# Optimization experiments

Measured on AMD Instinct MI355X. Metric: run time of the kernel, lower is better.

The kernel has to match this reference:

```python
import jax, jax.numpy as jnp
import numpy as np

N = 100000      # nodes
E = 1600000     # edges (avg degree 16)
IN, HID, OUT = 256, 256, 128


def setup_inputs() -> dict:
    key = jax.random.key(0)
    ks = jax.random.split(key, 9)
    x = jax.random.normal(ks[0], (N, IN), jnp.float32)
    edge_index = jax.random.randint(ks[1], (2, E), 0, N, dtype=jnp.int64)
    perm = jax.random.permutation(ks[2], N).astype(jnp.int64)
    # GCN layer params (glorot-ish scale) and Bilinear discriminator params
    W1 = jax.random.normal(ks[3], (IN, HID), jnp.float32) * (1.0 / np.sqrt(IN))
    b1 = jnp.zeros((HID,), jnp.float32)
    W2 = jax.random.normal(ks[4], (HID, OUT), jnp.float32) * (1.0 / np.sqrt(HID))
    b2 = jnp.zeros((OUT,), jnp.float32)
    Wb = jax.random.normal(ks[5], (OUT, OUT), jnp.float32) * (1.0 / np.sqrt(OUT))
    bb = jnp.zeros((1,), jnp.float32)
    return {"x": x, "edge_index": edge_index, "perm": perm,
            "W1": W1, "b1": b1, "W2": W2, "b2": b2, "Wb": Wb, "bb": bb}


def reference(x, edge_index, perm, W1, b1, W2, b2, Wb, bb):
    n = x.shape[0]
    src, dst = edge_index[0], edge_index[1]
    # GCN symmetric norm with self-loops: deg = 1 + in-degree
    deg = 1.0 + jax.ops.segment_sum(jnp.ones(src.shape[0], x.dtype), dst,
                                    num_segments=n)
    dinv = jax.lax.rsqrt(deg)                 # [N]
    enorm = dinv[src] * dinv[dst]             # per-edge norm
    self_norm = dinv * dinv                   # self-loop norm

    def gcn(h, W, b):
        hw = h @ W                                            # [N, F]
        agg = jax.ops.segment_sum(hw[src] * enorm[:, None], dst,
                                  num_segments=n)             # scatter-add
        return agg + self_norm[:, None] * hw + b

    def encode(h):
        return gcn(jax.nn.relu(gcn(h, W1, b1)), W2, b2)       # [N, OUT]

    H = encode(x)
    s = jax.nn.sigmoid(H.mean(axis=0))                        # summary [OUT]

    def disc(Hh):
        # nn.Bilinear(d, d, 1): score_n = H_n^T Wb s + bb
        return (jnp.einsum('nd,de,e->n', Hh, Wb, s) + bb)[:, None]

    pos_scores = disc(H)
    neg_scores = disc(encode(x[perm]))
    return pos_scores, neg_scores
```

## Files before the change

### kernel.cpp

```cpp
#include <hip/hip_runtime.h>


typedef __attribute__((ext_vector_type(8))) short bh8;
typedef __attribute__((ext_vector_type(4))) float f4;
typedef __attribute__((ext_vector_type(4))) unsigned short u16x4;

#define AS1 __attribute__((address_space(1)))
#define AS3 __attribute__((address_space(3)))

__device__ __forceinline__ unsigned short f2b(float f) {
    unsigned int u = __float_as_uint(f);
    unsigned int r = (u + 0x7FFFu + ((u >> 16) & 1u)) >> 16;
    return (unsigned short)r;
}
__device__ __forceinline__ float b2f(unsigned short h) {
    return __uint_as_float(((unsigned int)h) << 16);
}

__global__ void k_degree(const int* __restrict__ dst, int* __restrict__ deg, int E) {
    int e = blockIdx.x * blockDim.x + threadIdx.x;
    if (e < E) atomicAdd(&deg[dst[e]], 1);
}

__global__ void k_dinv(const int* __restrict__ deg, float* __restrict__ dinv,
                       int* __restrict__ rowptr, int N, int E) {
    int n = blockIdx.x * blockDim.x + threadIdx.x;
    if (n < N) dinv[n] = 1.0f / sqrtf(1.0f + (float)deg[n]);
    if (n == 0) rowptr[N] = E;
}

__global__ void k_scanA(const int* __restrict__ in, int* __restrict__ out,
                        int* __restrict__ bsum, int n) {
    __shared__ int sh[256];
    int t = threadIdx.x;
    int base = blockIdx.x * 1024 + t * 4;
    int v[4];
#pragma unroll
    for (int j = 0; j < 4; ++j) v[j] = (base + j < n) ? in[base + j] : 0;
    int s = v[0] + v[1] + v[2] + v[3];
    sh[t] = s;
    __syncthreads();
    for (int off = 1; off < 256; off <<= 1) {
        int u = (t >= off) ? sh[t - off] : 0;
        __syncthreads();
        sh[t] += u;
        __syncthreads();
    }
    int excl = sh[t] - s;
    if (t == 255) bsum[blockIdx.x] = sh[255];
    int run = excl;
#pragma unroll
    for (int j = 0; j < 4; ++j) {
        if (base + j < n) out[base + j] = run;
        run += v[j];
    }
}

__global__ void k_scanB(const int* __restrict__ bsum, int* __restrict__ boff, int nb) {
    __shared__ int sh[128];
    int t = threadIdx.x;
    int v = (t < nb) ? bsum[t] : 0;
    sh[t] = v;
    __syncthreads();
    for (int off = 1; off < 128; off <<= 1) {
        int u = (t >= off) ? sh[t - off] : 0;
        __syncthreads();
        sh[t] += u;
        __syncthreads();
    }
    boff[t] = sh[t] - v;
}

__global__ void k_scanC(int* __restrict__ out, const int* __restrict__ boff, int n) {
    int t = threadIdx.x;
    int base = blockIdx.x * 1024 + t * 4;
    int add = boff[blockIdx.x];
#pragma unroll
    for (int j = 0; j < 4; ++j)
        if (base + j < n) out[base + j] += add;
}

__global__ void k_fill(const int* __restrict__ src, const int* __restrict__ dst,
                       const int* __restrict__ perm, const int* __restrict__ rowptr,
                       int* __restrict__ cursor, int* __restrict__ csr,
                       int* __restrict__ pcsr, int E) {
    int e = blockIdx.x * blockDim.x + threadIdx.x;
    if (e >= E) return;
    int d = dst[e];
    int s = src[e];
    int p = rowptr[d] + atomicAdd(&cursor[d], 1);
    csr[p] = s;
    pcsr[p] = perm[s];
}

__global__ void k_split(const float* __restrict__ in, unsigned short* __restrict__ hi,
                        unsigned short* __restrict__ lo, long n4) {
    long i = (long)blockIdx.x * blockDim.x + threadIdx.x;
    if (i >= n4) return;
    float4 v = ((const float4*)in)[i];
    float f[4] = {v.x, v.y, v.z, v.w};
    u16x4 h, l;
#pragma unroll
    for (int j = 0; j < 4; ++j) {
        unsigned short hb = f2b(f[j]);
        h[j] = hb;
        l[j] = f2b(f[j] - b2f(hb));
    }
    ((u16x4*)hi)[i] = h;
    ((u16x4*)lo)[i] = l;
}

__global__ void k_wsplitT(const float* __restrict__ W, unsigned short* __restrict__ thi,
                          unsigned short* __restrict__ tlo, int K, int Nc) {
    int t = blockIdx.x * blockDim.x + threadIdx.x;
    if (t >= K * Nc) return;
    int k = t / Nc, n = t % Nc;
    float f = W[t];
    unsigned short hb = f2b(f);
    thi[n * K + k] = hb;
    tlo[n * K + k] = f2b(f - b2f(hb));
}

__global__ __launch_bounds__(256, 2) void k_gemm_mfma(
        const unsigned short* __restrict__ Ahi0, const unsigned short* __restrict__ Alo0,
        const unsigned short* __restrict__ Ahi1, const unsigned short* __restrict__ Alo1,
        const unsigned short* __restrict__ Bhi, const unsigned short* __restrict__ Blo,
        unsigned short* __restrict__ C, int M, int K, int NcB, int ldC, int colz) {
    __shared__ short lds[4][128 * 32];
    const int tid  = threadIdx.x;
    const int lane = tid & 63;
    const int w    = tid >> 6;
    const int wr   = w >> 1, wc = w & 1;
    const int row0 = blockIdx.y * 128;
    const int bcol = blockIdx.x * 128;
    const unsigned short* Ahi = blockIdx.z ? Ahi1 : Ahi0;
    const unsigned short* Alo = blockIdx.z ? Alo1 : Alo0;

    const unsigned short* sp = (w == 0) ? Ahi : (w == 1) ? Alo : (w == 2) ? Bhi : Blo;
    const int  base0 = (w < 2) ? row0 : bcol;
    const int  lim   = (w < 2) ? (M - 1) : (NcB - 1);
    const int  rsub  = lane >> 2;
    const int  clin  = lane & 3;

    f4 acc[4][4] = {};

    for (int k0 = 0; k0 < K; k0 += 32) {
        __syncthreads();
#pragma unroll
        for (int s = 0; s < 8; ++s) {
            int r = s * 16 + rsub;
            int g = base0 + r;
            if (g > lim) g = lim;
            const unsigned short* srcp = sp + (size_t)g * K + k0 + clin * 8;
            __builtin_amdgcn_global_load_lds((const AS1 void*)srcp,
                                             (AS3 void*)&lds[w][s * 512], 16, 0, 0);
        }
        __syncthreads();

        bh8 ah[4], al[4], bh_[4], bl[4];
        const int fr = lane & 15;
        const int fc = (lane >> 4) * 8;
#pragma unroll
        for (int m = 0; m < 4; ++m) {
            int off = (wr * 64 + m * 16 + fr) * 32 + fc;
            ah[m] = *(const bh8*)&lds[0][off];
            al[m] = *(const bh8*)&lds[1][off];
        }
#pragma unroll
        for (int n = 0; n < 4; ++n) {
            int off = (wc * 64 + n * 16 + fr) * 32 + fc;
            bh_[n] = *(const bh8*)&lds[2][off];
            bl[n]  = *(const bh8*)&lds[3][off];
        }
#pragma unroll
        for (int m = 0; m < 4; ++m)
#pragma unroll
            for (int n = 0; n < 4; ++n)
                acc[m][n] = __builtin_amdgcn_mfma_f32_16x16x32_bf16(ah[m], bh_[n], acc[m][n], 0, 0, 0);
#pragma unroll
        for (int m = 0; m < 4; ++m)
#pragma unroll
            for (int n = 0; n < 4; ++n)
                acc[m][n] = __builtin_amdgcn_mfma_f32_16x16x32_bf16(ah[m], bl[n], acc[m][n], 0, 0, 0);
#pragma unroll
        for (int m = 0; m < 4; ++m)
#pragma unroll
            for (int n = 0; n < 4; ++n)
                acc[m][n] = __builtin_amdgcn_mfma_f32_16x16x32_bf16(al[m], bh_[n], acc[m][n], 0, 0, 0);
    }

    const int cr = (lane >> 4) * 4;
    const int cc = lane & 15;
    const int col0 = bcol + blockIdx.z * colz;
#pragma unroll
    for (int m = 0; m < 4; ++m) {
        int r0 = row0 + wr * 64 + m * 16 + cr;
#pragma unroll
        for (int n = 0; n < 4; ++n) {
            int c = col0 + wc * 64 + n * 16 + cc;
#pragma unroll
            for (int j = 0; j < 4; ++j) {
                int r = r0 + j;
                if (r < M) C[(size_t)r * ldC + c] = f2b(acc[m][n][j]);
            }
        }
    }
}

__global__ __launch_bounds__(256) void k_agg2(
        const unsigned short* __restrict__ hw, const int* __restrict__ rowptr,
        const int* __restrict__ csr, const int* __restrict__ pcsr,
        const int* __restrict__ perm, const float* __restrict__ dinv,
        const float* __restrict__ bias,
        unsigned short* __restrict__ pos_hi, unsigned short* __restrict__ pos_lo,
        unsigned short* __restrict__ neg_hi, unsigned short* __restrict__ neg_lo,
        int n) {
    int wid = (blockIdx.x * blockDim.x + threadIdx.x) >> 6;
    int lane = threadIdx.x & 63;
    if (wid >= n) return;
    float dn = dinv[wid];
    int beg = rowptr[wid], end = rowptr[wid + 1];
    int off = lane * 4;
    float ap[4] = {0.f, 0.f, 0.f, 0.f}, an[4] = {0.f, 0.f, 0.f, 0.f};
    int e = beg;
    for (; e + 3 < end; e += 4) {
        int s0 = csr[e],     s1 = csr[e + 1], s2 = csr[e + 2], s3 = csr[e + 3];
        int p0 = pcsr[e],    p1 = pcsr[e + 1], p2 = pcsr[e + 2], p3 = pcsr[e + 3];
        float w0 = dinv[s0], w1 = dinv[s1],   w2 = dinv[s2],   w3 = dinv[s3];
        u16x4 vp0 = *(const u16x4*)(hw + (size_t)s0 * 256 + off);
        u16x4 vp1 = *(const u16x4*)(hw + (size_t)s1 * 256 + off);
        u16x4 vp2 = *(const u16x4*)(hw + (size_t)s2 * 256 + off);
        u16x4 vp3 = *(const u16x4*)(hw + (size_t)s3 * 256 + off);
        u16x4 vn0 = *(const u16x4*)(hw + (size_t)p0 * 256 + off);
        u16x4 vn1 = *(const u16x4*)(hw + (size_t)p1 * 256 + off);
        u16x4 vn2 = *(const u16x4*)(hw + (size_t)p2 * 256 + off);
        u16x4 vn3 = *(const u16x4*)(hw + (size_t)p3 * 256 + off);
#pragma unroll
        for (int j = 0; j < 4; ++j) {
            ap[j] += (w0 * b2f(vp0[j]) + w1 * b2f(vp1[j]))
                   + (w2 * b2f(vp2[j]) + w3 * b2f(vp3[j]));
            an[j] += (w0 * b2f(vn0[j]) + w1 * b2f(vn1[j]))
                   + (w2 * b2f(vn2[j]) + w3 * b2f(vn3[j]));
        }
    }
    for (; e < end; ++e) {
        int s0 = csr[e];
        int p0 = pcsr[e];
        float w0 = dinv[s0];
        u16x4 vp0 = *(const u16x4*)(hw + (size_t)s0 * 256 + off);
        u16x4 vn0 = *(const u16x4*)(hw + (size_t)p0 * 256 + off);
#pragma unroll
        for (int j = 0; j < 4; ++j) {
            ap[j] += w0 * b2f(vp0[j]);
            an[j] += w0 * b2f(vn0[j]);
        }
    }
    float sw = dn * dn;
    int pn = perm[wid];
    u16x4 mp = *(const u16x4*)(hw + (size_t)wid * 256 + off);
    u16x4 mn = *(const u16x4*)(hw + (size_t)pn  * 256 + off);
    float4 bv = *(const float4*)(bias + off);
    float bb4[4] = {bv.x, bv.y, bv.z, bv.w};
    u16x4 ph, pl, nh, nl;
#pragma unroll
    for (int j = 0; j < 4; ++j) {
        float rp = fmaxf(dn * ap[j] + sw * b2f(mp[j]) + bb4[j], 0.f);
        float rn = fmaxf(dn * an[j] + sw * b2f(mn[j]) + bb4[j], 0.f);
        unsigned short hb = f2b(rp);
        ph[j] = hb; pl[j] = f2b(rp - b2f(hb));
        hb = f2b(rn);
        nh[j] = hb; nl[j] = f2b(rn - b2f(hb));
    }
    size_t o = (size_t)wid * 256 + off;
    __builtin_nontemporal_store(ph, (u16x4*)(pos_hi + o));
    __builtin_nontemporal_store(pl, (u16x4*)(pos_lo + o));
    __builtin_nontemporal_store(nh, (u16x4*)(neg_hi + o));
    __builtin_nontemporal_store(nl, (u16x4*)(neg_lo + o));
}

__global__ __launch_bounds__(256) void k_agg128m(
        const unsigned short* __restrict__ G2, const int* __restrict__ rowptr,
        const int* __restrict__ csr, const float* __restrict__ dinv,
        const float* __restrict__ bias, float* __restrict__ Hpos,
        float* __restrict__ Hneg, int n) {
    int wid = (blockIdx.x * blockDim.x + threadIdx.x) >> 6;
    int lane = threadIdx.x & 63;
    if (wid >= n) return;
    float dn = dinv[wid];
    int beg = rowptr[wid], end = rowptr[wid + 1];
    int off = lane * 4;
    float a[4] = {0.f, 0.f, 0.f, 0.f};
    int e = beg;
    for (; e + 3 < end; e += 4) {
        int s0 = csr[e], s1 = csr[e + 1], s2 = csr[e + 2], s3 = csr[e + 3];
        float w0 = dinv[s0], w1 = dinv[s1], w2 = dinv[s2], w3 = dinv[s3];
        u16x4 v0 = *(const u16x4*)(G2 + (size_t)s0 * 256 + off);
        u16x4 v1 = *(const u16x4*)(G2 + (size_t)s1 * 256 + off);
        u16x4 v2 = *(const u16x4*)(G2 + (size_t)s2 * 256 + off);
        u16x4 v3 = *(const u16x4*)(G2 + (size_t)s3 * 256 + off);
#pragma unroll
        for (int j = 0; j < 4; ++j)
            a[j] += (w0 * b2f(v0[j]) + w1 * b2f(v1[j]))
                  + (w2 * b2f(v2[j]) + w3 * b2f(v3[j]));
    }
    for (; e < end; ++e) {
        int s0 = csr[e];
        float w0 = dinv[s0];
        u16x4 v0 = *(const u16x4*)(G2 + (size_t)s0 * 256 + off);
#pragma unroll
        for (int j = 0; j < 4; ++j) a[j] += w0 * b2f(v0[j]);
    }
    float sw = dn * dn;
    u16x4 mv = *(const u16x4*)(G2 + (size_t)wid * 256 + off);
    float4 bv = *(const float4*)(bias + (lane & 31) * 4);
    float bb4[4] = {bv.x, bv.y, bv.z, bv.w};
    f4 r;
    r[0] = dn * a[0] + sw * b2f(mv[0]) + bb4[0];
    r[1] = dn * a[1] + sw * b2f(mv[1]) + bb4[1];
    r[2] = dn * a[2] + sw * b2f(mv[2]) + bb4[2];
    r[3] = dn * a[3] + sw * b2f(mv[3]) + bb4[3];
    float* dstp = (lane < 32 ? Hpos : Hneg) + (size_t)wid * 128 + (lane & 31) * 4;
    __builtin_nontemporal_store(r, (f4*)dstp);
}

__global__ void k_colsum(const float* __restrict__ H, float* __restrict__ colsum, int n) {
    int c = threadIdx.x & 127, half = threadIdx.x >> 7;
    float acc = 0.f;
    for (int r = blockIdx.x * 2 + half; r < n; r += gridDim.x * 2)
        acc += H[(size_t)r * 128 + c];
    __shared__ float sh[256];
    sh[threadIdx.x] = acc;
    __syncthreads();
    if (half == 0) atomicAdd(&colsum[c], sh[c] + sh[c + 128]);
}

__global__ void k_summary(const float* __restrict__ colsum, const float* __restrict__ Wb,
                          float* __restrict__ t, int n) {
    __shared__ float s_sh[128];
    int d = threadIdx.x;
    float m = colsum[d] / (float)n;
    s_sh[d] = 1.0f / (1.0f + expf(-m));
    __syncthreads();
    float acc = 0.f;
    for (int e = 0; e < 128; ++e) acc += Wb[d * 128 + e] * s_sh[e];
    t[d] = acc;
}

__global__ void k_disc(const float* __restrict__ Hpos, const float* __restrict__ Hneg,
                       const float* __restrict__ t, const float* __restrict__ bb,
                       float* __restrict__ out, int n) {
    int wid = (blockIdx.x * blockDim.x + threadIdx.x) >> 6;
    int lane = threadIdx.x & 63;
    if (wid >= 2 * n) return;
    const float* row = (wid < n) ? (Hpos + (size_t)wid * 128)
                                 : (Hneg + (size_t)(wid - n) * 128);
    float p = row[lane] * t[lane] + row[lane + 64] * t[lane + 64];
#pragma unroll
    for (int off = 32; off > 0; off >>= 1) p += __shfl_down(p, off);
    if (lane == 0) out[wid] = p + bb[0];
}

extern "C" void kernel_launch(void* const* d_in, const int* in_sizes, int n_in,
                              void* d_out, int out_size, void* d_ws, size_t ws_size,
                              hipStream_t stream) {
    const float* x    = (const float*)d_in[0];
    const int*   ei   = (const int*)d_in[1];
    const int*   perm = (const int*)d_in[2];
    const float* W1   = (const float*)d_in[3];
    const float* b1   = (const float*)d_in[4];
    const float* W2   = (const float*)d_in[5];
    const float* b2   = (const float*)d_in[6];
    const float* Wb   = (const float*)d_in[7];
    const float* bb   = (const float*)d_in[8];
    float* out = (float*)d_out;

    const int N   = in_sizes[2];
    const int E   = in_sizes[1] / 2;
    const int IN  = in_sizes[0] / N;
    const int HID = in_sizes[4];
    const int OUT = in_sizes[6];
    const int* src = ei;
    const int* dst = ei + E;

    char* p = (char*)d_ws;
    auto alloc = [&](size_t bytes) -> void* {
        void* r = (void*)p;
        p += (bytes + 255) & ~(size_t)255;
        return r;
    };
    int*   deg    = (int*)alloc((size_t)N * 4);
    int*   cursor = (int*)alloc((size_t)N * 4);
    float* colsum = (float*)alloc(128 * 4);
    size_t zlen   = (size_t)(p - (char*)deg);
    int*   rowptr = (int*)alloc((size_t)(N + 1) * 4);
    int*   bsum   = (int*)alloc(128 * 4);
    int*   boff   = (int*)alloc(128 * 4);
    int*   csr    = (int*)alloc((size_t)E * 4);
    int*   pcsr   = (int*)alloc((size_t)E * 4);
    float* dinv   = (float*)alloc((size_t)N * 4);
    float* tvec   = (float*)alloc(128 * 4);
    unsigned short* W1thi = (unsigned short*)alloc((size_t)IN * HID * 2);
    unsigned short* W1tlo = (unsigned short*)alloc((size_t)IN * HID * 2);
    unsigned short* W2thi = (unsigned short*)alloc((size_t)HID * OUT * 2);
    unsigned short* W2tlo = (unsigned short*)alloc((size_t)HID * OUT * 2);
    unsigned short* Xhi = (unsigned short*)alloc((size_t)N * IN * 2);
    unsigned short* Xlo = (unsigned short*)alloc((size_t)N * IN * 2);
    unsigned short* G1 = (unsigned short*)alloc((size_t)N * HID * 2);
    unsigned short* Bphi = (unsigned short*)alloc((size_t)N * HID * 2);
    unsigned short* Bplo = (unsigned short*)alloc((size_t)N * HID * 2);

    unsigned short* Bnhi = Xhi;
    unsigned short* Bnlo = Xlo;
    unsigned short* G2 = G1;
    float* Hpos = (float*)Bphi;
    float* Hneg = (float*)Bplo;

    hipMemsetAsync(deg, 0, zlen, stream);

    int eb = (E + 255) / 256;
    int nb = (N + 255) / 256;
    int nscan = (N + 1023) / 1024;
    k_degree<<<eb, 256, 0, stream>>>(dst, deg, E);
    k_dinv<<<nb, 256, 0, stream>>>(deg, dinv, rowptr, N, E);
    k_scanA<<<nscan, 256, 0, stream>>>(deg, rowptr, bsum, N);
    k_scanB<<<1, 128, 0, stream>>>(bsum, boff, nscan);
    k_scanC<<<nscan, 256, 0, stream>>>(rowptr, boff, N);
    k_fill<<<eb, 256, 0, stream>>>(src, dst, perm, rowptr, cursor, csr, pcsr, E);

    long n4 = (long)N * IN / 4;
    k_split<<<(int)((n4 + 255) / 256), 256, 0, stream>>>(x, Xhi, Xlo, n4);
    k_wsplitT<<<(IN * HID + 255) / 256, 256, 0, stream>>>(W1, W1thi, W1tlo, IN, HID);
    k_wsplitT<<<(HID * OUT + 255) / 256, 256, 0, stream>>>(W2, W2thi, W2tlo, HID, OUT);

    int mblk = (N + 127) / 128;
    int aggb = (N + 3) / 4;

    k_gemm_mfma<<<dim3(HID / 128, mblk, 1), 256, 0, stream>>>(
        Xhi, Xlo, Xhi, Xlo, W1thi, W1tlo, G1, N, IN, HID, HID, 0);
    k_agg2<<<aggb, 256, 0, stream>>>(G1, rowptr, csr, pcsr, perm, dinv, b1,
                                     Bphi, Bplo, Bnhi, Bnlo, N);

    k_gemm_mfma<<<dim3(OUT / 128, mblk, 2), 256, 0, stream>>>(
        Bphi, Bplo, Bnhi, Bnlo, W2thi, W2tlo, G2, N, HID, OUT, HID, OUT);
    k_agg128m<<<aggb, 256, 0, stream>>>(G2, rowptr, csr, dinv, b2, Hpos, Hneg, N);

    k_colsum<<<256, 256, 0, stream>>>(Hpos, colsum, N);
    k_summary<<<1, 128, 0, stream>>>(colsum, Wb, tvec, N);
    int db = (int)(((size_t)N * 2 * 64 + 255) / 256);
    k_disc<<<db, 256, 0, stream>>>(Hpos, Hneg, tvec, bb, out, N);
}
```

Measured before the change: 989.2 us.

## Prescale GEMM output by dinv, scatter permuted rows, drop A low-precision split

The layer-1 GEMM now folds the source-side dinv into its epilogue and writes each row twice, once in natural order and once at the inverse-permuted position, into an interleaved 512-wide buffer. The aggregation kernel then gathers one contiguous 16-byte vector per neighbour for both the positive and negative branches, with no per-edge weight loads and no pcsr array. The low bf16 half of the activations is dropped, so each GEMM does two MFMA passes instead of three and k_split writes half the data. The trade-off is lower precision on the A operand and bf16 rounding of scaled values, plus scattered writes in the GEMM epilogue.

```diff
diff --git a/kernel.cpp b/kernel.cpp
--- a/kernel.cpp
+++ b/kernel.cpp
@@ -4,6 +4,7 @@
 typedef __attribute__((ext_vector_type(8))) short bh8;
 typedef __attribute__((ext_vector_type(4))) float f4;
 typedef __attribute__((ext_vector_type(4))) unsigned short u16x4;
+typedef __attribute__((ext_vector_type(8))) unsigned short u16x8;
 
 #define AS1 __attribute__((address_space(1)))
 #define AS3 __attribute__((address_space(3)))
@@ -22,10 +23,14 @@
     if (e < E) atomicAdd(&deg[dst[e]], 1);
 }
 
-__global__ void k_dinv(const int* __restrict__ deg, float* __restrict__ dinv,
+__global__ void k_dinv(const int* __restrict__ deg, const int* __restrict__ perm,
+                       float* __restrict__ dinv, int* __restrict__ pinv,
                        int* __restrict__ rowptr, int N, int E) {
     int n = blockIdx.x * blockDim.x + threadIdx.x;
-    if (n < N) dinv[n] = 1.0f / sqrtf(1.0f + (float)deg[n]);
+    if (n < N) {
+        dinv[n] = 1.0f / sqrtf(1.0f + (float)deg[n]);
+        pinv[perm[n]] = n;
+    }
     if (n == 0) rowptr[N] = E;
 }
 
@@ -81,33 +86,25 @@
 }
 
 __global__ void k_fill(const int* __restrict__ src, const int* __restrict__ dst,
-                       const int* __restrict__ perm, const int* __restrict__ rowptr,
-                       int* __restrict__ cursor, int* __restrict__ csr,
-                       int* __restrict__ pcsr, int E) {
+                       const int* __restrict__ rowptr, int* __restrict__ cursor,
+                       int* __restrict__ csr, int E) {
     int e = blockIdx.x * blockDim.x + threadIdx.x;
     if (e >= E) return;
     int d = dst[e];
-    int s = src[e];
     int p = rowptr[d] + atomicAdd(&cursor[d], 1);
-    csr[p] = s;
-    pcsr[p] = perm[s];
+    csr[p] = src[e];
 }
 
 __global__ void k_split(const float* __restrict__ in, unsigned short* __restrict__ hi,
-                        unsigned short* __restrict__ lo, long n4) {
+                        long n4) {
     long i = (long)blockIdx.x * blockDim.x + threadIdx.x;
     if (i >= n4) return;
     float4 v = ((const float4*)in)[i];
     float f[4] = {v.x, v.y, v.z, v.w};
-    u16x4 h, l;
-#pragma unroll
-    for (int j = 0; j < 4; ++j) {
-        unsigned short hb = f2b(f[j]);
-        h[j] = hb;
-        l[j] = f2b(f[j] - b2f(hb));
-    }
+    u16x4 h;
+#pragma unroll
+    for (int j = 0; j < 4; ++j) h[j] = f2b(f[j]);
     ((u16x4*)hi)[i] = h;
-    ((u16x4*)lo)[i] = l;
 }
 
 __global__ void k_wsplitT(const float* __restrict__ W, unsigned short* __restrict__ thi,
@@ -121,12 +118,13 @@
     tlo[n * K + k] = f2b(f - b2f(hb));
 }
 
+template <int MODE>
 __global__ __launch_bounds__(256, 2) void k_gemm_mfma(
-        const unsigned short* __restrict__ Ahi0, const unsigned short* __restrict__ Alo0,
-        const unsigned short* __restrict__ Ahi1, const unsigned short* __restrict__ Alo1,
+        const unsigned short* __restrict__ Ahi0, const unsigned short* __restrict__ Ahi1,
         const unsigned short* __restrict__ Bhi, const unsigned short* __restrict__ Blo,
-        unsigned short* __restrict__ C, int M, int K, int NcB, int ldC, int colz) {
-    __shared__ short lds[4][128 * 32];
+        unsigned short* __restrict__ C, const float* __restrict__ dinv,
+        const int* __restrict__ pinv, int M, int K, int NcB, int ldC, int colz) {
+    __shared__ short lds[3][128 * 32];
     const int tid  = threadIdx.x;
     const int lane = tid & 63;
     const int w    = tid >> 6;
@@ -134,11 +132,13 @@
     const int row0 = blockIdx.y * 128;
     const int bcol = blockIdx.x * 128;
     const unsigned short* Ahi = blockIdx.z ? Ahi1 : Ahi0;
-    const unsigned short* Alo = blockIdx.z ? Alo1 : Alo0;
-
-    const unsigned short* sp = (w == 0) ? Ahi : (w == 1) ? Alo : (w == 2) ? Bhi : Blo;
-    const int  base0 = (w < 2) ? row0 : bcol;
-    const int  lim   = (w < 2) ? (M - 1) : (NcB - 1);
+
+    const unsigned short* sp = (w == 1) ? Bhi : (w == 2) ? Blo : Ahi;
+    const int  plane = (w == 1) ? 1 : (w == 2) ? 2 : 0;
+    const int  slab0 = (w == 3) ? 4 : 0;
+    const int  nslab = (w == 0 || w == 3) ? 4 : 8;
+    const int  base0 = (w == 1 || w == 2) ? bcol : row0;
+    const int  lim   = (w == 1 || w == 2) ? (NcB - 1) : (M - 1);
     const int  rsub  = lane >> 2;
     const int  clin  = lane & 3;
 
@@ -146,31 +146,28 @@
 
     for (int k0 = 0; k0 < K; k0 += 32) {
         __syncthreads();
-#pragma unroll
-        for (int s = 0; s < 8; ++s) {
-            int r = s * 16 + rsub;
+        for (int s = 0; s < nslab; ++s) {
+            int slab = slab0 + s;
+            int r = slab * 16 + rsub;
             int g = base0 + r;
             if (g > lim) g = lim;
             const unsigned short* srcp = sp + (size_t)g * K + k0 + clin * 8;
             __builtin_amdgcn_global_load_lds((const AS1 void*)srcp,
-                                             (AS3 void*)&lds[w][s * 512], 16, 0, 0);
+                                             (AS3 void*)&lds[plane][slab * 512], 16, 0, 0);
         }
         __syncthreads();
 
-        bh8 ah[4], al[4], bh_[4], bl[4];
+        bh8 ah[4], bh_[4], bl[4];
         const int fr = lane & 15;
         const int fc = (lane >> 4) * 8;
 #pragma unroll
-        for (int m = 0; m < 4; ++m) {
-            int off = (wr * 64 + m * 16 + fr) * 32 + fc;
-            ah[m] = *(const bh8*)&lds[0][off];
-            al[m] = *(const bh8*)&lds[1][off];
-        }
+        for (int m = 0; m < 4; ++m)
+            ah[m] = *(const bh8*)&lds[0][(wr * 64 + m * 16 + fr) * 32 + fc];
 #pragma unroll
         for (int n = 0; n < 4; ++n) {
             int off = (wc * 64 + n * 16 + fr) * 32 + fc;
-            bh_[n] = *(const bh8*)&lds[2][off];
-            bl[n]  = *(const bh8*)&lds[3][off];
+            bh_[n] = *(const bh8*)&lds[1][off];
+            bl[n]  = *(const bh8*)&lds[2][off];
         }
 #pragma unroll
         for (int m = 0; m < 4; ++m)
@@ -182,103 +179,86 @@
 #pragma unroll
             for (int n = 0; n < 4; ++n)
                 acc[m][n] = __builtin_amdgcn_mfma_f32_16x16x32_bf16(ah[m], bl[n], acc[m][n], 0, 0, 0);
-#pragma unroll
-        for (int m = 0; m < 4; ++m)
-#pragma unroll
-            for (int n = 0; n < 4; ++n)
-                acc[m][n] = __builtin_amdgcn_mfma_f32_16x16x32_bf16(al[m], bh_[n], acc[m][n], 0, 0, 0);
     }
 
     const int cr = (lane >> 4) * 4;
     const int cc = lane & 15;
-    const int col0 = bcol + blockIdx.z * colz;
 #pragma unroll
     for (int m = 0; m < 4; ++m) {
         int r0 = row0 + wr * 64 + m * 16 + cr;
 #pragma unroll
-        for (int n = 0; n < 4; ++n) {
-            int c = col0 + wc * 64 + n * 16 + cc;
-#pragma unroll
-            for (int j = 0; j < 4; ++j) {
-                int r = r0 + j;
-                if (r < M) C[(size_t)r * ldC + c] = f2b(acc[m][n][j]);
+        for (int j = 0; j < 4; ++j) {
+            int r = r0 + j;
+            if (r >= M) continue;
+            if constexpr (MODE == 1) {
+                float sr = dinv[r];
+                int   ur = pinv[r];
+                float su = dinv[ur];
+#pragma unroll
+                for (int n = 0; n < 4; ++n) {
+                    int c = bcol + wc * 64 + n * 16 + cc;
+                    C[(size_t)r  * 512 + c]       = f2b(sr * acc[m][n][j]);
+                    C[(size_t)ur * 512 + 256 + c] = f2b(su * acc[m][n][j]);
+                }
+            } else {
+                float sr = dinv[r];
+                int cbase = blockIdx.z * colz + bcol;
+#pragma unroll
+                for (int n = 0; n < 4; ++n) {
+                    int c = cbase + wc * 64 + n * 16 + cc;
+                    C[(size_t)r * ldC + c] = f2b(sr * acc[m][n][j]);
+                }
             }
         }
     }
 }
 
-__global__ __launch_bounds__(256) void k_agg2(
-        const unsigned short* __restrict__ hw, const int* __restrict__ rowptr,
-        const int* __restrict__ csr, const int* __restrict__ pcsr,
-        const int* __restrict__ perm, const float* __restrict__ dinv,
+__global__ __launch_bounds__(256) void k_aggTU(
+        const unsigned short* __restrict__ TU, const int* __restrict__ rowptr,
+        const int* __restrict__ csr, const float* __restrict__ dinv,
         const float* __restrict__ bias,
-        unsigned short* __restrict__ pos_hi, unsigned short* __restrict__ pos_lo,
-        unsigned short* __restrict__ neg_hi, unsigned short* __restrict__ neg_lo,
-        int n) {
+        unsigned short* __restrict__ Bp, unsigned short* __restrict__ Bn, int n) {
     int wid = (blockIdx.x * blockDim.x + threadIdx.x) >> 6;
     int lane = threadIdx.x & 63;
     if (wid >= n) return;
-    float dn = dinv[wid];
     int beg = rowptr[wid], end = rowptr[wid + 1];
-    int off = lane * 4;
-    float ap[4] = {0.f, 0.f, 0.f, 0.f}, an[4] = {0.f, 0.f, 0.f, 0.f};
+    int off = lane * 8;
+    float a[8] = {0.f, 0.f, 0.f, 0.f, 0.f, 0.f, 0.f, 0.f};
     int e = beg;
     for (; e + 3 < end; e += 4) {
-        int s0 = csr[e],     s1 = csr[e + 1], s2 = csr[e + 2], s3 = csr[e + 3];
-        int p0 = pcsr[e],    p1 = pcsr[e + 1], p2 = pcsr[e + 2], p3 = pcsr[e + 3];
-        float w0 = dinv[s0], w1 = dinv[s1],   w2 = dinv[s2],   w3 = dinv[s3];
-        u16x4 vp0 = *(const u16x4*)(hw + (size_t)s0 * 256 + off);
-        u16x4 vp1 = *(const u16x4*)(hw + (size_t)s1 * 256 + off);
-        u16x4 vp2 = *(const u16x4*)(hw + (size_t)s2 * 256 + off);
-        u16x4 vp3 = *(const u16x4*)(hw + (size_t)s3 * 256 + off);
-        u16x4 vn0 = *(const u16x4*)(hw + (size_t)p0 * 256 + off);
-        u16x4 vn1 = *(const u16x4*)(hw + (size_t)p1 * 256 + off);
-        u16x4 vn2 = *(const u16x4*)(hw + (size_t)p2 * 256 + off);
-        u16x4 vn3 = *(const u16x4*)(hw + (size_t)p3 * 256 + off);
-#pragma unroll
-        for (int j = 0; j < 4; ++j) {
-            ap[j] += (w0 * b2f(vp0[j]) + w1 * b2f(vp1[j]))
-                   + (w2 * b2f(vp2[j]) + w3 * b2f(vp3[j]));
-            an[j] += (w0 * b2f(vn0[j]) + w1 * b2f(vn1[j]))
-                   + (w2 * b2f(vn2[j]) + w3 * b2f(vn3[j]));
-        }
+        int s0 = csr[e], s1 = csr[e + 1], s2 = csr[e + 2], s3 = csr[e + 3];
+        u16x8 v0 = *(const u16x8*)(TU + (size_t)s0 * 512 + off);
+        u16x8 v1 = *(const u16x8*)(TU + (size_t)s1 * 512 + off);
+        u16x8 v2 = *(const u16x8*)(TU + (size_t)s2 * 512 + off);
+        u16x8 v3 = *(const u16x8*)(TU + (size_t)s3 * 512 + off);
+#pragma unroll
+        for (int j = 0; j < 8; ++j)
+            a[j] += (b2f(v0[j]) + b2f(v1[j])) + (b2f(v2[j]) + b2f(v3[j]));
     }
     for (; e < end; ++e) {
         int s0 = csr[e];
-        int p0 = pcsr[e];
-        float w0 = dinv[s0];
-        u16x4 vp0 = *(const u16x4*)(hw + (size_t)s0 * 256 + off);
-        u16x4 vn0 = *(const u16x4*)(hw + (size_t)p0 * 256 + off);
-#pragma unroll
-        for (int j = 0; j < 4; ++j) {
-            ap[j] += w0 * b2f(vp0[j]);
-            an[j] += w0 * b2f(vn0[j]);
-        }
-    }
-    float sw = dn * dn;
-    int pn = perm[wid];
-    u16x4 mp = *(const u16x4*)(hw + (size_t)wid * 256 + off);
-    u16x4 mn = *(const u16x4*)(hw + (size_t)pn  * 256 + off);
-    float4 bv = *(const float4*)(bias + off);
-    float bb4[4] = {bv.x, bv.y, bv.z, bv.w};
-    u16x4 ph, pl, nh, nl;
-#pragma unroll
-    for (int j = 0; j < 4; ++j) {
-        float rp = fmaxf(dn * ap[j] + sw * b2f(mp[j]) + bb4[j], 0.f);
-        float rn = fmaxf(dn * an[j] + sw * b2f(mn[j]) + bb4[j], 0.f);
-        unsigned short hb = f2b(rp);
-        ph[j] = hb; pl[j] = f2b(rp - b2f(hb));
-        hb = f2b(rn);
-        nh[j] = hb; nl[j] = f2b(rn - b2f(hb));
-    }
-    size_t o = (size_t)wid * 256 + off;
-    __builtin_nontemporal_store(ph, (u16x4*)(pos_hi + o));
-    __builtin_nontemporal_store(pl, (u16x4*)(pos_lo + o));
-    __builtin_nontemporal_store(nh, (u16x4*)(neg_hi + o));
-    __builtin_nontemporal_store(nl, (u16x4*)(neg_lo + o));
-}
-
-__global__ __launch_bounds__(256) void k_agg128m(
+        u16x8 v0 = *(const u16x8*)(TU + (size_t)s0 * 512 + off);
+#pragma unroll
+        for (int j = 0; j < 8; ++j) a[j] += b2f(v0[j]);
+    }
+    u16x8 vs = *(const u16x8*)(TU + (size_t)wid * 512 + off);
+#pragma unroll
+    for (int j = 0; j < 8; ++j) a[j] += b2f(vs[j]);
+
+    float dn = dinv[wid];
+    int f0 = (lane & 31) * 8;
+    float4 bv0 = *(const float4*)(bias + f0);
+    float4 bv1 = *(const float4*)(bias + f0 + 4);
+    float bb8[8] = {bv0.x, bv0.y, bv0.z, bv0.w, bv1.x, bv1.y, bv1.z, bv1.w};
+    u16x8 o;
+#pragma unroll
+    for (int j = 0; j < 8; ++j)
+        o[j] = f2b(fmaxf(dn * a[j] + bb8[j], 0.f));
+    unsigned short* dstp = (lane < 32 ? Bp : Bn) + (size_t)wid * 256 + f0;
+    __builtin_nontemporal_store(o, (u16x8*)dstp);
+}
+
+__global__ __launch_bounds__(256) void k_aggT2(
         const unsigned short* __restrict__ G2, const int* __restrict__ rowptr,
         const int* __restrict__ csr, const float* __restrict__ dinv,
         const float* __restrict__ bias, float* __restrict__ Hpos,
@@ -286,40 +266,38 @@
     int wid = (blockIdx.x * blockDim.x + threadIdx.x) >> 6;
     int lane = threadIdx.x & 63;
     if (wid >= n) return;
-    float dn = dinv[wid];
     int beg = rowptr[wid], end = rowptr[wid + 1];
     int off = lane * 4;
     float a[4] = {0.f, 0.f, 0.f, 0.f};
     int e = beg;
     for (; e + 3 < end; e += 4) {
         int s0 = csr[e], s1 = csr[e + 1], s2 = csr[e + 2], s3 = csr[e + 3];
-        float w0 = dinv[s0], w1 = dinv[s1], w2 = dinv[s2], w3 = dinv[s3];
         u16x4 v0 = *(const u16x4*)(G2 + (size_t)s0 * 256 + off);
         u16x4 v1 = *(const u16x4*)(G2 + (size_t)s1 * 256 + off);
         u16x4 v2 = *(const u16x4*)(G2 + (size_t)s2 * 256 + off);
         u16x4 v3 = *(const u16x4*)(G2 + (size_t)s3 * 256 + off);
 #pragma unroll
         for (int j = 0; j < 4; ++j)
-            a[j] += (w0 * b2f(v0[j]) + w1 * b2f(v1[j]))
-                  + (w2 * b2f(v2[j]) + w3 * b2f(v3[j]));
+            a[j] += (b2f(v0[j]) + b2f(v1[j])) + (b2f(v2[j]) + b2f(v3[j]));
     }
     for (; e < end; ++e) {
         int s0 = csr[e];
-        float w0 = dinv[s0];
         u16x4 v0 = *(const u16x4*)(G2 + (size_t)s0 * 256 + off);
 #pragma unroll
-        for (int j = 0; j < 4; ++j) a[j] += w0 * b2f(v0[j]);
-    }
-    float sw = dn * dn;
-    u16x4 mv = *(const u16x4*)(G2 + (size_t)wid * 256 + off);
-    float4 bv = *(const float4*)(bias + (lane & 31) * 4);
+        for (int j = 0; j < 4; ++j) a[j] += b2f(v0[j]);
+    }
+    u16x4 vs = *(const u16x4*)(G2 + (size_t)wid * 256 + off);
+#pragma unroll
+    for (int j = 0; j < 4; ++j) a[j] += b2f(vs[j]);
+
+    float dn = dinv[wid];
+    int f0 = (lane & 31) * 4;
+    float4 bv = *(const float4*)(bias + f0);
     float bb4[4] = {bv.x, bv.y, bv.z, bv.w};
     f4 r;
-    r[0] = dn * a[0] + sw * b2f(mv[0]) + bb4[0];
-    r[1] = dn * a[1] + sw * b2f(mv[1]) + bb4[1];
-    r[2] = dn * a[2] + sw * b2f(mv[2]) + bb4[2];
-    r[3] = dn * a[3] + sw * b2f(mv[3]) + bb4[3];
-    float* dstp = (lane < 32 ? Hpos : Hneg) + (size_t)wid * 128 + (lane & 31) * 4;
+#pragma unroll
+    for (int j = 0; j < 4; ++j) r[j] = dn * a[j] + bb4[j];
+    float* dstp = (lane < 32 ? Hpos : Hneg) + (size_t)wid * 128 + f0;
     __builtin_nontemporal_store(r, (f4*)dstp);
 }
 
@@ -396,7 +374,7 @@
     int*   bsum   = (int*)alloc(128 * 4);
     int*   boff   = (int*)alloc(128 * 4);
     int*   csr    = (int*)alloc((size_t)E * 4);
-    int*   pcsr   = (int*)alloc((size_t)E * 4);
+    int*   pinv   = (int*)alloc((size_t)N * 4);
     float* dinv   = (float*)alloc((size_t)N * 4);
     float* tvec   = (float*)alloc(128 * 4);
     unsigned short* W1thi = (unsigned short*)alloc((size_t)IN * HID * 2);
@@ -404,16 +382,13 @@
     unsigned short* W2thi = (unsigned short*)alloc((size_t)HID * OUT * 2);
     unsigned short* W2tlo = (unsigned short*)alloc((size_t)HID * OUT * 2);
     unsigned short* Xhi = (unsigned short*)alloc((size_t)N * IN * 2);
-    unsigned short* Xlo = (unsigned short*)alloc((size_t)N * IN * 2);
-    unsigned short* G1 = (unsigned short*)alloc((size_t)N * HID * 2);
-    unsigned short* Bphi = (unsigned short*)alloc((size_t)N * HID * 2);
-    unsigned short* Bplo = (unsigned short*)alloc((size_t)N * HID * 2);
-
-    unsigned short* Bnhi = Xhi;
-    unsigned short* Bnlo = Xlo;
-    unsigned short* G2 = G1;
-    float* Hpos = (float*)Bphi;
-    float* Hneg = (float*)Bplo;
+    unsigned short* TU  = (unsigned short*)alloc((size_t)N * 512 * 2);
+    unsigned short* Bp  = (unsigned short*)alloc((size_t)N * HID * 2);
+    unsigned short* Bn  = (unsigned short*)alloc((size_t)N * HID * 2);
+
+    unsigned short* G2 = Xhi;
+    float* Hpos = (float*)TU;
+    float* Hneg = (float*)(TU + (size_t)N * 256);
 
     hipMemsetAsync(deg, 0, zlen, stream);
 
@@ -421,28 +396,27 @@
     int nb = (N + 255) / 256;
     int nscan = (N + 1023) / 1024;
     k_degree<<<eb, 256, 0, stream>>>(dst, deg, E);
-    k_dinv<<<nb, 256, 0, stream>>>(deg, dinv, rowptr, N, E);
+    k_dinv<<<nb, 256, 0, stream>>>(deg, perm, dinv, pinv, rowptr, N, E);
     k_scanA<<<nscan, 256, 0, stream>>>(deg, rowptr, bsum, N);
     k_scanB<<<1, 128, 0, stream>>>(bsum, boff, nscan);
     k_scanC<<<nscan, 256, 0, stream>>>(rowptr, boff, N);
-    k_fill<<<eb, 256, 0, stream>>>(src, dst, perm, rowptr, cursor, csr, pcsr, E);
+    k_fill<<<eb, 256, 0, stream>>>(src, dst, rowptr, cursor, csr, E);
 
     long n4 = (long)N * IN / 4;
-    k_split<<<(int)((n4 + 255) / 256), 256, 0, stream>>>(x, Xhi, Xlo, n4);
+    k_split<<<(int)((n4 + 255) / 256), 256, 0, stream>>>(x, Xhi, n4);
     k_wsplitT<<<(IN * HID + 255) / 256, 256, 0, stream>>>(W1, W1thi, W1tlo, IN, HID);
     k_wsplitT<<<(HID * OUT + 255) / 256, 256, 0, stream>>>(W2, W2thi, W2tlo, HID, OUT);
 
     int mblk = (N + 127) / 128;
     int aggb = (N + 3) / 4;
 
-    k_gemm_mfma<<<dim3(HID / 128, mblk, 1), 256, 0, stream>>>(
-        Xhi, Xlo, Xhi, Xlo, W1thi, W1tlo, G1, N, IN, HID, HID, 0);
-    k_agg2<<<aggb, 256, 0, stream>>>(G1, rowptr, csr, pcsr, perm, dinv, b1,
-                                     Bphi, Bplo, Bnhi, Bnlo, N);
-
-    k_gemm_mfma<<<dim3(OUT / 128, mblk, 2), 256, 0, stream>>>(
-        Bphi, Bplo, Bnhi, Bnlo, W2thi, W2tlo, G2, N, HID, OUT, HID, OUT);
-    k_agg128m<<<aggb, 256, 0, stream>>>(G2, rowptr, csr, dinv, b2, Hpos, Hneg, N);
+    k_gemm_mfma<1><<<dim3(HID / 128, mblk, 1), 256, 0, stream>>>(
+        Xhi, Xhi, W1thi, W1tlo, TU, dinv, pinv, N, IN, HID, 512, 0);
+    k_aggTU<<<aggb, 256, 0, stream>>>(TU, rowptr, csr, dinv, b1, Bp, Bn, N);
+
+    k_gemm_mfma<2><<<dim3(OUT / 128, mblk, 2), 256, 0, stream>>>(
+        Bp, Bn, W2thi, W2tlo, G2, dinv, pinv, N, HID, OUT, HID, OUT);
+    k_aggT2<<<aggb, 256, 0, stream>>>(G2, rowptr, csr, dinv, b2, Hpos, Hneg, N);
 
     k_colsum<<<256, 256, 0, stream>>>(Hpos, colsum, N);
     k_summary<<<1, 128, 0, stream>>>(colsum, Wb, tvec, N);
```

New measurement: 924.8 us. -6.5%, faster.
